# Performance work log

Measured on AMD Instinct MI355X. Metric: run time of the kernel, lower is better.

## Reference

```python
import jax, jax.numpy as jnp
import numpy as np

N = 50000      # nodes
E = 1600000    # edges
IN = 128       # in_features
OUT = 64       # out_features
H = 2          # heads
ALPHA = 0.2    # LeakyReLU negative slope


def setup_inputs() -> dict:
    key = jax.random.key(0)
    k1, k2, k3, k4 = jax.random.split(key, 4)
    x = jax.random.normal(k1, (N, IN), dtype=jnp.float32)
    edge_index = jax.random.randint(k2, (2, E), 0, N, dtype=jnp.int32)
    # xavier-uniform-ish scaled params
    W = jax.random.normal(k3, (H, IN, OUT), dtype=jnp.float32) / np.float32(np.sqrt(IN))
    a = jax.random.normal(k4, (H, 2 * OUT, 1), dtype=jnp.float32) * np.float32(0.1)
    return {"x": x, "W": W, "a": a, "edge_index": edge_index}


def reference(x, W, a, edge_index):
    src = edge_index[0]
    dst = edge_index[1]
    # per-head linear transform: [N, H, O]
    Wh = jnp.einsum('ni,hio->nho', x, W)
    # split attention vector: a @ [Wh_i || Wh_j] == Wh_i@a_i + Wh_j@a_j
    a_i = a[:, :OUT, 0]   # [H, O]
    a_j = a[:, OUT:, 0]   # [H, O]
    s_i = jnp.einsum('nho,ho->nh', Wh, a_i)   # [N, H]
    s_j = jnp.einsum('nho,ho->nh', Wh, a_j)   # [N, H]
    # per-edge attention logits, LeakyReLU
    e = jax.nn.leaky_relu(s_i[src] + s_j[dst], negative_slope=ALPHA)  # [E, H]
    # faithful to source: GLOBAL softmax over all edges (dim=0) per head
    attn = jax.nn.softmax(e, axis=0)  # [E, H]
    # dropout with rate 0.0 -> identity (eval mode)
    msg = attn[:, :, None] * Wh[dst]  # [E, H, O]
    h = jax.ops.segment_sum(msg, dst, num_segments=N)  # [N, H, O]
    # concat heads along feature dim
    return h.reshape(N, H * OUT)
```

## Files before the change

### kernel.cpp

```cpp
#include <hip/hip_runtime.h>

#define NN 50000
#define EE 1600000
#define INF 128
#define OUTF 64
#define NH 2
#define ALPHA 0.2f

#define RNG 16
#define NPR (NN / RNG)
#define NBB 256
#define EPB (EE / NBB)
#define BCAP 640
#define NBNODE 391

typedef __attribute__((ext_vector_type(8))) short s16x8;
typedef __attribute__((ext_vector_type(4))) float f32x4;

__device__ __forceinline__ unsigned short bf16_rne(float f) {
    union { float f; unsigned u; } v; v.f = f;
    unsigned r = v.u + 0x7FFFu + ((v.u >> 16) & 1u);
    return (unsigned short)(r >> 16);
}
__device__ __forceinline__ float bf16_val(unsigned short h) {
    union { unsigned u; float f; } v; v.u = ((unsigned)h) << 16;
    return v.f;
}
__device__ __forceinline__ void split8(const float4 a, const float4 b,
                                       s16x8& hi, s16x8& lo) {
    const float p[8] = {a.x, a.y, a.z, a.w, b.x, b.y, b.z, b.w};
    #pragma unroll
    for (int j = 0; j < 8; ++j) {
        const unsigned short h = bf16_rne(p[j]);
        hi[j] = (short)h;
        lo[j] = (short)bf16_rne(p[j] - bf16_val(h));
    }
}


__global__ __launch_bounds__(256)
void gat_wprep(const float* __restrict__ Wg, const float* __restrict__ a,
               unsigned short* __restrict__ Wf, float* __restrict__ Z)
{
    const int tid = threadIdx.x;
    const int idx = blockIdx.x * 256 + tid;
    if (idx < 2) Z[idx] = 0.0f;
    {
        const int h = idx >> 13;
        const int k = (idx >> 6) & 127;
        const int o = idx & 63;
        const float w = Wg[idx];
        const unsigned short hi = bf16_rne(w);
        const unsigned short lo = bf16_rne(w - bf16_val(hi));
        const int n  = h * 64 + o;
        const int nt = n >> 4;
        const int ks = k >> 5;
        const int kk = k & 31;
        const int ln = (kk >> 3) * 16 + (n & 15);
        const int pos = ((nt * 4 + ks) * 64 + ln) * 8 + (kk & 7);
        Wf[pos] = hi;
        Wf[18432 + pos] = lo;
    }
    if (blockIdx.x == 0) {
        for (int i = tid; i < 2048; i += 256) {
            Wf[16384 + i] = 0;
            Wf[18432 + 16384 + i] = 0;
        }
        __syncthreads();
        if (tid < 128) {
            const int k = tid;
            float u[4] = {0.f, 0.f, 0.f, 0.f};
            for (int o = 0; o < 64; ++o) {
                const float w0 = Wg[k * 64 + o];
                const float w1 = Wg[8192 + k * 64 + o];
                u[0] = fmaf(w0, a[o], u[0]);
                u[1] = fmaf(w0, a[64 + o], u[1]);
                u[2] = fmaf(w1, a[128 + o], u[2]);
                u[3] = fmaf(w1, a[192 + o], u[3]);
            }
            const int ks = k >> 5;
            const int kk = k & 31;
            #pragma unroll
            for (int n = 0; n < 4; ++n) {
                const int ln = (kk >> 3) * 16 + n;
                const int pos = ((32 + ks) * 64 + ln) * 8 + (kk & 7);
                const unsigned short hi = bf16_rne(u[n]);
                Wf[pos] = hi;
                Wf[18432 + pos] = bf16_rne(u[n] - bf16_val(hi));
            }
        }
    }
}

__global__ __launch_bounds__(256)
void gat_node(const float* __restrict__ x, const unsigned short* __restrict__ Wf,
              const int* __restrict__ ei, float* __restrict__ out,
              float* __restrict__ si, float* __restrict__ sj,
              unsigned* __restrict__ buckets, int* __restrict__ counts)
{
    __shared__ int cnt[16];
    const int tid = threadIdx.x;

    if (blockIdx.x >= NBNODE) {
        const int bid = blockIdx.x - NBNODE;
        if (tid < 16) cnt[tid] = 0;
        __syncthreads();
        const int e0 = bid * EPB;
        for (int i = tid; i < EPB; i += 256) {
            const int d = ei[EE + e0 + i];
            const int s = ei[e0 + i];
            const int r = d / NPR;
            const int rel = d - r * NPR;
            const int pos = atomicAdd(&cnt[r], 1);
            if (pos < BCAP)
                buckets[(r * NBB + bid) * BCAP + pos] =
                    (unsigned)s | ((unsigned)rel << 16);
        }
        __syncthreads();
        if (tid < 16) counts[tid * NBB + bid] = min(cnt[tid], BCAP);
        return;
    }

    const int lane = tid & 63;
    const int wv = tid >> 6;
    const int lm = lane & 15;
    const int quad = lane >> 4;

    const int rowA0 = blockIdx.x * 128 + wv * 32 + lm;
    const int rowA1 = rowA0 + 16;
    const int rc0 = rowA0 < NN ? rowA0 : NN - 1;
    const int rc1 = rowA1 < NN ? rowA1 : NN - 1;
    const float* xp0 = x + (size_t)rc0 * INF + quad * 8;
    const float* xp1 = x + (size_t)rc1 * INF + quad * 8;

    f32x4 acc[2][9];
    #pragma unroll
    for (int mi = 0; mi < 2; ++mi)
        #pragma unroll
        for (int nt = 0; nt < 9; ++nt) acc[mi][nt] = (f32x4)0.0f;

    #pragma unroll
    for (int ks = 0; ks < 4; ++ks) {
        s16x8 ah0, al0, ah1, al1;
        {
            const float4 u0 = *(const float4*)(xp0 + ks * 32);
            const float4 v0 = *(const float4*)(xp0 + ks * 32 + 4);
            split8(u0, v0, ah0, al0);
            const float4 u1 = *(const float4*)(xp1 + ks * 32);
            const float4 v1 = *(const float4*)(xp1 + ks * 32 + 4);
            split8(u1, v1, ah1, al1);
        }
        #pragma unroll
        for (int nt = 0; nt < 9; ++nt) {
            const s16x8 bh = *(const s16x8*)&Wf[((nt * 4 + ks) * 64 + lane) * 8];
            const s16x8 bl = *(const s16x8*)&Wf[18432 + ((nt * 4 + ks) * 64 + lane) * 8];
            acc[0][nt] = __builtin_amdgcn_mfma_f32_16x16x32_bf16(ah0, bh, acc[0][nt], 0, 0, 0);
            acc[0][nt] = __builtin_amdgcn_mfma_f32_16x16x32_bf16(ah0, bl, acc[0][nt], 0, 0, 0);
            acc[0][nt] = __builtin_amdgcn_mfma_f32_16x16x32_bf16(al0, bh, acc[0][nt], 0, 0, 0);
            acc[1][nt] = __builtin_amdgcn_mfma_f32_16x16x32_bf16(ah1, bh, acc[1][nt], 0, 0, 0);
            acc[1][nt] = __builtin_amdgcn_mfma_f32_16x16x32_bf16(ah1, bl, acc[1][nt], 0, 0, 0);
            acc[1][nt] = __builtin_amdgcn_mfma_f32_16x16x32_bf16(al1, bh, acc[1][nt], 0, 0, 0);
        }
    }

    #pragma unroll
    for (int mi = 0; mi < 2; ++mi) {
        const int rowb = blockIdx.x * 128 + wv * 32 + mi * 16 + quad * 4;
        #pragma unroll
        for (int r = 0; r < 4; ++r) {
            const int rr = rowb + r;
            if (rr < NN) {
                const float sv = acc[mi][8][r];
                if (lm == 0)      si[2 * rr] = sv;
                else if (lm == 1) sj[2 * rr] = sv;
                else if (lm == 2) si[2 * rr + 1] = sv;
                else if (lm == 3) sj[2 * rr + 1] = sv;
                float* orow = out + (size_t)rr * (NH * OUTF) + lm;
                #pragma unroll
                for (int nt = 0; nt < 8; ++nt) orow[nt * 16] = acc[mi][nt][r];
            }
        }
    }
}

__global__ __launch_bounds__(512)
void gat_hist(const unsigned* __restrict__ buckets, const int* __restrict__ counts,
              const float* __restrict__ si, const float* __restrict__ sj,
              float* __restrict__ partial, float* __restrict__ Z)
{
    __shared__ float bins[NPR * 2];
    __shared__ float zr0[8], zr1[8];
    const int c = blockIdx.x;
    const int r = blockIdx.y;
    const int nlo = r * NPR;

    for (int i = threadIdx.x; i < NPR; i += 512)
        ((float2*)bins)[i] = make_float2(0.f, 0.f);
    __syncthreads();

    float z0 = 0.f, z1 = 0.f;
    #pragma unroll
    for (int bb = 0; bb < 8; ++bb) {
        const int b = c * 8 + bb;
        const int n = counts[r * NBB + b];
        const unsigned* seg = buckets + (size_t)(r * NBB + b) * BCAP;
        for (int i = threadIdx.x; i < n; i += 512) {
            const unsigned pk = seg[i];
            const int s = (int)(pk & 0xFFFFu);
            const int rel = (int)(pk >> 16);
            const float2 vi = *(const float2*)&si[2 * s];
            const float2 vj = *(const float2*)&sj[2 * (nlo + rel)];
            float a0 = vi.x + vj.x; a0 = a0 > 0.f ? a0 : ALPHA * a0;
            float a1 = vi.y + vj.y; a1 = a1 > 0.f ? a1 : ALPHA * a1;
            const float w0 = expf(a0);
            const float w1 = expf(a1);
            atomicAdd(&bins[2 * rel], w0);
            atomicAdd(&bins[2 * rel + 1], w1);
            z0 += w0; z1 += w1;
        }
    }

    #pragma unroll
    for (int m = 1; m < 64; m <<= 1) {
        z0 += __shfl_xor(z0, m, 64);
        z1 += __shfl_xor(z1, m, 64);
    }
    const int wv = threadIdx.x >> 6;
    if ((threadIdx.x & 63) == 0) { zr0[wv] = z0; zr1[wv] = z1; }
    __syncthreads();
    if (threadIdx.x == 0) {
        float t0 = 0.f, t1 = 0.f;
        #pragma unroll
        for (int i = 0; i < 8; ++i) { t0 += zr0[i]; t1 += zr1[i]; }
        atomicAdd(&Z[0], t0);
        atomicAdd(&Z[1], t1);
    }

    float2* P = (float2*)(partial + (size_t)c * 100000 + nlo * 2);
    for (int i = threadIdx.x; i < NPR; i += 512)
        P[i] = ((const float2*)bins)[i];
}

__global__ __launch_bounds__(256)
void gat_scale(float* __restrict__ out, const float* __restrict__ partial,
               const float* __restrict__ Z)
{
    __shared__ float sc[256];
    const int tid = threadIdx.x;
    const int n0 = blockIdx.x * 128;
    const float rz0 = 1.0f / Z[0];
    const float rz1 = 1.0f / Z[1];

    const int nvals = min(256, 100000 - n0 * 2);
    if (tid < nvals) {
        float ssum = 0.f;
        #pragma unroll 8
        for (int c = 0; c < 32; ++c)
            ssum += partial[(size_t)c * 100000 + n0 * 2 + tid];
        sc[tid] = ssum * ((tid & 1) ? rz1 : rz0);
    }
    __syncthreads();

    float4* ob = (float4*)(out + (size_t)n0 * 128);
    const int lim4 = min(128, NN - n0) * 32;
    for (int i = tid; i < lim4; i += 256) {
        const int row = i >> 5;
        const int c4 = i & 31;
        const float s = sc[row * 2 + (c4 >> 4)];
        float4 v = ob[i];
        v.x *= s; v.y *= s; v.z *= s; v.w *= s;
        ob[i] = v;
    }
}

extern "C" void kernel_launch(void* const* d_in, const int* in_sizes, int n_in,
                              void* d_out, int out_size, void* d_ws, size_t ws_size,
                              hipStream_t stream)
{
    const float* x = (const float*)d_in[0];
    const float* W = (const float*)d_in[1];
    const float* a = (const float*)d_in[2];
    const int* ei = (const int*)d_in[3];
    float* out = (float*)d_out;
    float* ws = (float*)d_ws;

    float* si = ws;
    float* sj = ws + 100000;
    float* Z = ws + 200000;
    unsigned short* Wf = (unsigned short*)(ws + 200016);
    int* counts = (int*)(ws + 218448);
    unsigned* buckets = (unsigned*)(ws + 222560);
    float* partial = ws + 2844000;

    gat_wprep<<<dim3(64), dim3(256), 0, stream>>>(W, a, Wf, Z);

    gat_node<<<dim3(NBNODE + NBB), dim3(256), 0, stream>>>(x, Wf, ei, out, si, sj,
                                                           buckets, counts);

    gat_hist<<<dim3(32, RNG), dim3(512), 0, stream>>>(buckets, counts, si, sj,
                                                      partial, Z);

    gat_scale<<<dim3(NBNODE), dim3(256), 0, stream>>>(out, partial, Z);
}
```

Baseline: 162.0 us.

## Stage W fragments in LDS, vectorize edge loads, reorder bucketing blocks first

The node kernel now copies the prepared bf16 weight fragments (72 KB) into shared memory before the MFMA loop, replacing per-lane global reads. Edge bucketing blocks move ahead of the GEMM blocks and read the source and destination index arrays as int4. NBB changes to 250 so EPB divides evenly for the int4 loads, and the histogram pass reads packed bucket entries as uint4. Histogram chunking and the scale reduction follow the new chunk count. The large LDS allocation may cut occupancy of the GEMM blocks, and because the bucketing path shares that kernel its blocks may be limited as well.

```diff
diff --git a/kernel.cpp b/kernel.cpp
--- a/kernel.cpp
+++ b/kernel.cpp
@@ -9,10 +9,12 @@
 
 #define RNG 16
 #define NPR (NN / RNG)
-#define NBB 256
+#define NBB 250
 #define EPB (EE / NBB)
 #define BCAP 640
 #define NBNODE 391
+#define HCH 25
+#define SPB (NBB / HCH)
 
 typedef __attribute__((ext_vector_type(8))) short s16x8;
 typedef __attribute__((ext_vector_type(4))) float f32x4;
@@ -98,35 +100,50 @@
               float* __restrict__ si, float* __restrict__ sj,
               unsigned* __restrict__ buckets, int* __restrict__ counts)
 {
+    __shared__ unsigned short WsL[36864];
     __shared__ int cnt[16];
     const int tid = threadIdx.x;
 
-    if (blockIdx.x >= NBNODE) {
-        const int bid = blockIdx.x - NBNODE;
+    if (blockIdx.x < NBB) {
+        const int bid = blockIdx.x;
         if (tid < 16) cnt[tid] = 0;
         __syncthreads();
         const int e0 = bid * EPB;
-        for (int i = tid; i < EPB; i += 256) {
-            const int d = ei[EE + e0 + i];
-            const int s = ei[e0 + i];
-            const int r = d / NPR;
-            const int rel = d - r * NPR;
-            const int pos = atomicAdd(&cnt[r], 1);
-            if (pos < BCAP)
-                buckets[(r * NBB + bid) * BCAP + pos] =
-                    (unsigned)s | ((unsigned)rel << 16);
+        for (int i = tid; i < EPB / 4; i += 256) {
+            const int4 s4 = *(const int4*)&ei[e0 + 4 * i];
+            const int4 d4 = *(const int4*)&ei[EE + e0 + 4 * i];
+            const int ss[4] = {s4.x, s4.y, s4.z, s4.w};
+            const int dd[4] = {d4.x, d4.y, d4.z, d4.w};
+            #pragma unroll
+            for (int k = 0; k < 4; ++k) {
+                const int r = dd[k] / NPR;
+                const int rel = dd[k] - r * NPR;
+                const int pos = atomicAdd(&cnt[r], 1);
+                if (pos < BCAP)
+                    buckets[(size_t)(r * NBB + bid) * BCAP + pos] =
+                        (unsigned)ss[k] | ((unsigned)rel << 16);
+            }
         }
         __syncthreads();
         if (tid < 16) counts[tid * NBB + bid] = min(cnt[tid], BCAP);
         return;
     }
 
+    const int bx = blockIdx.x - NBB;
     const int lane = tid & 63;
     const int wv = tid >> 6;
     const int lm = lane & 15;
     const int quad = lane >> 4;
 
-    const int rowA0 = blockIdx.x * 128 + wv * 32 + lm;
+    {
+        const float4* gsrc = (const float4*)Wf;
+        float4* ldst = (float4*)WsL;
+        #pragma unroll
+        for (int i = 0; i < 18; ++i)
+            ldst[i * 256 + tid] = gsrc[i * 256 + tid];
+    }
+
+    const int rowA0 = bx * 128 + wv * 32 + lm;
     const int rowA1 = rowA0 + 16;
     const int rc0 = rowA0 < NN ? rowA0 : NN - 1;
     const int rc1 = rowA1 < NN ? rowA1 : NN - 1;
@@ -138,6 +155,8 @@
     for (int mi = 0; mi < 2; ++mi)
         #pragma unroll
         for (int nt = 0; nt < 9; ++nt) acc[mi][nt] = (f32x4)0.0f;
+
+    __syncthreads();
 
     #pragma unroll
     for (int ks = 0; ks < 4; ++ks) {
@@ -152,8 +171,8 @@
         }
         #pragma unroll
         for (int nt = 0; nt < 9; ++nt) {
-            const s16x8 bh = *(const s16x8*)&Wf[((nt * 4 + ks) * 64 + lane) * 8];
-            const s16x8 bl = *(const s16x8*)&Wf[18432 + ((nt * 4 + ks) * 64 + lane) * 8];
+            const s16x8 bh = *(const s16x8*)&WsL[((nt * 4 + ks) * 64 + lane) * 8];
+            const s16x8 bl = *(const s16x8*)&WsL[18432 + ((nt * 4 + ks) * 64 + lane) * 8];
             acc[0][nt] = __builtin_amdgcn_mfma_f32_16x16x32_bf16(ah0, bh, acc[0][nt], 0, 0, 0);
             acc[0][nt] = __builtin_amdgcn_mfma_f32_16x16x32_bf16(ah0, bl, acc[0][nt], 0, 0, 0);
             acc[0][nt] = __builtin_amdgcn_mfma_f32_16x16x32_bf16(al0, bh, acc[0][nt], 0, 0, 0);
@@ -165,7 +184,7 @@
 
     #pragma unroll
     for (int mi = 0; mi < 2; ++mi) {
-        const int rowb = blockIdx.x * 128 + wv * 32 + mi * 16 + quad * 4;
+        const int rowb = bx * 128 + wv * 32 + mi * 16 + quad * 4;
         #pragma unroll
         for (int r = 0; r < 4; ++r) {
             const int rr = rowb + r;
@@ -200,23 +219,31 @@
 
     float z0 = 0.f, z1 = 0.f;
     #pragma unroll
-    for (int bb = 0; bb < 8; ++bb) {
-        const int b = c * 8 + bb;
+    for (int bb = 0; bb < SPB; ++bb) {
+        const int b = c * SPB + bb;
         const int n = counts[r * NBB + b];
-        const unsigned* seg = buckets + (size_t)(r * NBB + b) * BCAP;
-        for (int i = threadIdx.x; i < n; i += 512) {
-            const unsigned pk = seg[i];
-            const int s = (int)(pk & 0xFFFFu);
-            const int rel = (int)(pk >> 16);
-            const float2 vi = *(const float2*)&si[2 * s];
-            const float2 vj = *(const float2*)&sj[2 * (nlo + rel)];
-            float a0 = vi.x + vj.x; a0 = a0 > 0.f ? a0 : ALPHA * a0;
-            float a1 = vi.y + vj.y; a1 = a1 > 0.f ? a1 : ALPHA * a1;
-            const float w0 = expf(a0);
-            const float w1 = expf(a1);
-            atomicAdd(&bins[2 * rel], w0);
-            atomicAdd(&bins[2 * rel + 1], w1);
-            z0 += w0; z1 += w1;
+        const uint4* seg4 = (const uint4*)(buckets + (size_t)(r * NBB + b) * BCAP);
+        const int n4 = (n + 3) >> 2;
+        for (int i = threadIdx.x; i < n4; i += 512) {
+            const uint4 pk4 = seg4[i];
+            const unsigned pks[4] = {pk4.x, pk4.y, pk4.z, pk4.w};
+            #pragma unroll
+            for (int j = 0; j < 4; ++j) {
+                if (4 * i + j < n) {
+                    const unsigned pk = pks[j];
+                    const int s = (int)(pk & 0xFFFFu);
+                    const int rel = (int)(pk >> 16);
+                    const float2 vi = *(const float2*)&si[2 * s];
+                    const float2 vj = *(const float2*)&sj[2 * (nlo + rel)];
+                    float a0 = vi.x + vj.x; a0 = a0 > 0.f ? a0 : ALPHA * a0;
+                    float a1 = vi.y + vj.y; a1 = a1 > 0.f ? a1 : ALPHA * a1;
+                    const float w0 = expf(a0);
+                    const float w1 = expf(a1);
+                    atomicAdd(&bins[2 * rel], w0);
+                    atomicAdd(&bins[2 * rel + 1], w1);
+                    z0 += w0; z1 += w1;
+                }
+            }
         }
     }
 
@@ -254,8 +281,8 @@
     const int nvals = min(256, 100000 - n0 * 2);
     if (tid < nvals) {
         float ssum = 0.f;
-        #pragma unroll 8
-        for (int c = 0; c < 32; ++c)
+        #pragma unroll 5
+        for (int c = 0; c < HCH; ++c)
             ssum += partial[(size_t)c * 100000 + n0 * 2 + tid];
         sc[tid] = ssum * ((tid & 1) ? rz1 : rz0);
     }
@@ -289,16 +316,16 @@
     float* Z = ws + 200000;
     unsigned short* Wf = (unsigned short*)(ws + 200016);
     int* counts = (int*)(ws + 218448);
-    unsigned* buckets = (unsigned*)(ws + 222560);
-    float* partial = ws + 2844000;
+    unsigned* buckets = (unsigned*)(ws + 222464);
+    float* partial = ws + 2782464;
 
     gat_wprep<<<dim3(64), dim3(256), 0, stream>>>(W, a, Wf, Z);
 
-    gat_node<<<dim3(NBNODE + NBB), dim3(256), 0, stream>>>(x, Wf, ei, out, si, sj,
+    gat_node<<<dim3(NBB + NBNODE), dim3(256), 0, stream>>>(x, Wf, ei, out, si, sj,
                                                            buckets, counts);
 
-    gat_hist<<<dim3(32, RNG), dim3(512), 0, stream>>>(buckets, counts, si, sj,
-                                                      partial, Z);
+    gat_hist<<<dim3(HCH, RNG), dim3(512), 0, stream>>>(buckets, counts, si, sj,
+                                                       partial, Z);
 
     gat_scale<<<dim3(NBNODE), dim3(256), 0, stream>>>(out, partial, Z);
 }
```

Measured after the change: 145.5 us. 1.11x faster.
